# Kernel tuning notes

Hardware: AMD Instinct MI355X
Metric: run time of the kernel (lower is better)

Reference implementation:

```python
import jax, jax.numpy as jnp
import numpy as np

N = 8192      # nodes
IN_FEATS = 128
OUT_FEATS = 64
DEG = 16      # avg degree for random edges
NEG_SLOPE = 0.01  # nn.LeakyReLU default


def setup_inputs() -> dict:
    key = jax.random.key(0)
    k1, k2, k3, k4, k5, k6 = jax.random.split(key, 6)
    inputs = jax.random.normal(k1, (N, IN_FEATS), dtype=jnp.float32)
    # Random symmetric adjacency with self-loops (dense, as in the original module)
    us = jax.random.randint(k2, (N * DEG,), 0, N)
    vs = jax.random.randint(k3, (N * DEG,), 0, N)
    A = jnp.zeros((N, N), dtype=jnp.float32)
    A = A.at[us, vs].set(1.0)
    A = A.at[vs, us].set(1.0)
    idx = jnp.arange(N)
    A = A.at[idx, idx].set(1.0)
    # Linear layer params (torch nn.Linear: weight [out, in])
    W = jax.random.normal(k4, (OUT_FEATS, IN_FEATS), dtype=jnp.float32) * (1.0 / np.sqrt(IN_FEATS))
    b = jnp.zeros((OUT_FEATS,), dtype=jnp.float32)
    # attention params, torch.rand -> uniform [0,1)
    a1 = jax.random.uniform(k5, (1, OUT_FEATS), dtype=jnp.float32)
    a2 = jax.random.uniform(k6, (1, OUT_FEATS), dtype=jnp.float32)
    return {"inputs": inputs, "A": A, "W": W, "b": b, "a1": a1, "a2": a2}


def reference(inputs, A, W, b, a1, a2):
    z = inputs @ W.T + b                                  # [N, out]
    zi = jnp.sum(a1 * z, axis=1, keepdims=True)           # [N, 1]
    zj = jnp.sum(a2 * z, axis=1, keepdims=True)           # [N, 1]
    n = A.shape[0]
    idx = jnp.arange(n)
    diagA = jnp.diagonal(A)                               # A_ii
    # attention_A + attention_B = A*zi + diag(A_ii * zj)  (A*(eye*zj) only keeps diagonal)
    att = A * zi
    att = att.at[idx, idx].add(diagA * zj[:, 0])
    att = jax.nn.leaky_relu(att, NEG_SLOPE)
    att = jnp.exp(att) * A
    att = att / jnp.sum(att, axis=1, keepdims=True)       # row-normalize
    h = z - att @ z
    return jax.nn.relu(h)
```

## Files before the change

### kernel.cpp

```cpp
#include <hip/hip_runtime.h>
#include <math.h>

#define NN 8192
#define IN_F 128
#define OUT_F 64
#define NEG_SLOPE 0.01f
#define K1_ROWS 8
#define CAP 256

__global__ __launch_bounds__(256, 4) void k1_linear(
    const float* __restrict__ X, const float* __restrict__ W,
    const float* __restrict__ b, const float* __restrict__ a1,
    const float* __restrict__ a2, float* __restrict__ z,
    float* __restrict__ ev, float* __restrict__ dv)
{
    __shared__ float Wl[OUT_F * 129];
    __shared__ float xs[K1_ROWS * IN_F];
    const int t = threadIdx.x;
    const int blk = blockIdx.x;

    for (int idx = t; idx < OUT_F * IN_F; idx += 256) {
        int f = idx >> 7, k = idx & 127;
        Wl[f * 129 + k] = W[idx];
    }
    {
        const float4* Xv = reinterpret_cast<const float4*>(X + (size_t)blk * (K1_ROWS * IN_F));
        float4* xsv = reinterpret_cast<float4*>(xs);
        if (t < K1_ROWS * IN_F / 4) xsv[t] = Xv[t];
    }
    __syncthreads();

    const int wid = t >> 6;
    const int lane = t & 63;
    const float bias = b[lane];
    const float a1f = a1[lane], a2f = a2[lane];

#pragma unroll
    for (int r2 = 0; r2 < 2; ++r2) {
        const int row = wid * 2 + r2;
        float acc = 0.f;
#pragma unroll 8
        for (int k = 0; k < IN_F; ++k)
            acc = fmaf(xs[row * IN_F + k], Wl[lane * 129 + k], acc);
        const float zval = acc + bias;
        const int i = blk * K1_ROWS + row;
        z[i * OUT_F + lane] = zval;

        float p1 = a1f * zval;
        float p2 = a2f * zval;
#pragma unroll
        for (int off = 32; off > 0; off >>= 1) {
            p1 += __shfl_down(p1, off, 64);
            p2 += __shfl_down(p2, off, 64);
        }
        if (lane == 0) {
            const float s1 = p1;
            const float s2 = p1 + p2;
            const float l1 = s1 > 0.f ? s1 : NEG_SLOPE * s1;
            const float l2 = s2 > 0.f ? s2 : NEG_SLOPE * s2;
            ev[i] = expf(l1);
            dv[i] = expf(l2);
        }
    }
}

__global__ __launch_bounds__(256, 8) void k2a_compress(
    const float* __restrict__ A, int* __restrict__ degi, int* __restrict__ nbr)
{
    __shared__ int lst[CAP];
    __shared__ int cnt;
    const int i = blockIdx.x;
    const int t = threadIdx.x;
    if (t == 0) cnt = 0;
    __syncthreads();

    const int4* __restrict__ Arow =
        reinterpret_cast<const int4*>(A + (size_t)i * NN);

    int4 b0 = Arow[0 * 256 + t];
    int4 b1 = Arow[1 * 256 + t];
    int4 b2 = Arow[2 * 256 + t];
    int4 b3 = Arow[3 * 256 + t];
    int4 b4 = Arow[4 * 256 + t];
    int4 b5 = Arow[5 * 256 + t];
    int4 b6 = Arow[6 * 256 + t];
    int4 b7 = Arow[7 * 256 + t];

#define STEP(S, B)                                                           \
    {                                                                        \
        const int base = ((S) * 256 + t) * 4;                                \
        if (B.x != 0) { int k = atomicAdd(&cnt, 1); if (k < CAP) lst[k] = base;     } \
        if (B.y != 0) { int k = atomicAdd(&cnt, 1); if (k < CAP) lst[k] = base + 1; } \
        if (B.z != 0) { int k = atomicAdd(&cnt, 1); if (k < CAP) lst[k] = base + 2; } \
        if (B.w != 0) { int k = atomicAdd(&cnt, 1); if (k < CAP) lst[k] = base + 3; } \
    }
    STEP(0, b0) STEP(1, b1) STEP(2, b2) STEP(3, b3)
    STEP(4, b4) STEP(5, b5) STEP(6, b6) STEP(7, b7)
#undef STEP

    __syncthreads();
    const int c = cnt;
    if (t == 0) degi[i] = c;
    if (t < c && t < CAP) nbr[(size_t)i * CAP + t] = lst[t];
}

__global__ __launch_bounds__(256, 8) void k2b_gather(
    const int* __restrict__ degi, const int* __restrict__ nbr,
    const float* __restrict__ z, const float* __restrict__ ev,
    const float* __restrict__ dv, float* __restrict__ out)
{
    const int t = threadIdx.x;
    const int wid = t >> 6, lane = t & 63;
    const int i = blockIdx.x * 4 + wid;

    const int cnt = degi[i];
    const int* rowl = nbr + (size_t)i * CAP;

    float acc = 0.f;
    for (int k0 = 0; k0 < cnt; k0 += 64) {
        const int m = (cnt - k0) < 64 ? (cnt - k0) : 64;
        const int jv = (lane < m) ? rowl[k0 + lane] : 0;
        int kk = 0;
        for (; kk + 4 <= m; kk += 4) {
            const int j0 = __shfl(jv, kk + 0, 64);
            const int j1 = __shfl(jv, kk + 1, 64);
            const int j2 = __shfl(jv, kk + 2, 64);
            const int j3 = __shfl(jv, kk + 3, 64);
            const float z0 = z[(size_t)j0 * OUT_F + lane];
            const float z1 = z[(size_t)j1 * OUT_F + lane];
            const float z2 = z[(size_t)j2 * OUT_F + lane];
            const float z3 = z[(size_t)j3 * OUT_F + lane];
            acc += (z0 + z1) + (z2 + z3);
        }
        for (; kk < m; ++kk) {
            const int j = __shfl(jv, kk, 64);
            acc += z[(size_t)j * OUT_F + lane];
        }
    }

    const float degT = (float)cnt;
    const float e = ev[i], d = dv[i];
    const float S = (degT - 1.f) * e + d;
    const float zif = z[(size_t)i * OUT_F + lane];
    const float h = zif * (1.f + (e - d) / S) - (e / S) * acc;
    out[(size_t)i * OUT_F + lane] = h > 0.f ? h : 0.f;
}

extern "C" void kernel_launch(void* const* d_in, const int* in_sizes, int n_in,
                              void* d_out, int out_size, void* d_ws, size_t ws_size,
                              hipStream_t stream) {
    const float* X  = (const float*)d_in[0];
    const float* A  = (const float*)d_in[1];
    const float* W  = (const float*)d_in[2];
    const float* b  = (const float*)d_in[3];
    const float* a1 = (const float*)d_in[4];
    const float* a2 = (const float*)d_in[5];
    float* out = (float*)d_out;

    char* ws = (char*)d_ws;
    float* z    = (float*)ws;
    float* ev   = (float*)(ws + (size_t)NN * OUT_F * 4);
    float* dv   = ev + NN;
    int*   degi = (int*)(dv + NN);
    int*   nbr  = degi + NN;

    k1_linear<<<NN / K1_ROWS, 256, 0, stream>>>(X, W, b, a1, a2, z, ev, dv);
    k2a_compress<<<NN, 256, 0, stream>>>(A, degi, nbr);
    k2b_gather<<<NN / 4, 256, 0, stream>>>(degi, nbr, z, ev, dv, out);
}
```

Before: 64.84 us.

## Fuse linear projection into adjacency compression kernel and use nontemporal A loads

Merges the linear layer and attention-scalar computation into the per-row adjacency compression kernel, so each block computes one row of z, split across four waves with a shared-memory reduction, while its A row loads are in flight. This drops a kernel launch and a serialisation point, hiding the small GEMM under the memory-bound scan of the dense 256 MB adjacency. A is now read with nontemporal loads to avoid polluting cache. In exchange, every block reloads its slice of W from global/L2, and launch bounds drop from 8 to 4 blocks per CU, which may reduce the occupancy available to the streaming loads.

```diff
diff --git a/kernel.cpp b/kernel.cpp
--- a/kernel.cpp
+++ b/kernel.cpp
@@ -5,49 +5,82 @@
 #define IN_F 128
 #define OUT_F 64
 #define NEG_SLOPE 0.01f
-#define K1_ROWS 8
 #define CAP 256
 
-__global__ __launch_bounds__(256, 4) void k1_linear(
-    const float* __restrict__ X, const float* __restrict__ W,
-    const float* __restrict__ b, const float* __restrict__ a1,
-    const float* __restrict__ a2, float* __restrict__ z,
-    float* __restrict__ ev, float* __restrict__ dv)
+typedef int v4i __attribute__((ext_vector_type(4)));
+
+__global__ __launch_bounds__(256, 4) void k2a_fused(
+    const float* __restrict__ A, const float* __restrict__ X,
+    const float* __restrict__ W, const float* __restrict__ b,
+    const float* __restrict__ a1, const float* __restrict__ a2,
+    float* __restrict__ z, float* __restrict__ ev, float* __restrict__ dv,
+    int* __restrict__ degi, int* __restrict__ nbr)
 {
-    __shared__ float Wl[OUT_F * 129];
-    __shared__ float xs[K1_ROWS * IN_F];
+    __shared__ float xs[IN_F];
+    __shared__ float pz[4][64];
+    __shared__ int lst[CAP];
+    __shared__ int cnt;
+
+    const int i = blockIdx.x;
     const int t = threadIdx.x;
-    const int blk = blockIdx.x;
+    const int wid = t >> 6, lane = t & 63;
 
-    for (int idx = t; idx < OUT_F * IN_F; idx += 256) {
-        int f = idx >> 7, k = idx & 127;
-        Wl[f * 129 + k] = W[idx];
-    }
-    {
-        const float4* Xv = reinterpret_cast<const float4*>(X + (size_t)blk * (K1_ROWS * IN_F));
-        float4* xsv = reinterpret_cast<float4*>(xs);
-        if (t < K1_ROWS * IN_F / 4) xsv[t] = Xv[t];
-    }
+    if (t == 0) cnt = 0;
+    if (t < 32)
+        reinterpret_cast<float4*>(xs)[t] =
+            reinterpret_cast<const float4*>(X + (size_t)i * IN_F)[t];
+
+    const float4* wp4 = reinterpret_cast<const float4*>(W) + (lane * 32 + wid * 8);
+    float4 w4[8];
+#pragma unroll
+    for (int q = 0; q < 8; ++q) w4[q] = wp4[q];
+
     __syncthreads();
 
-    const int wid = t >> 6;
-    const int lane = t & 63;
-    const float bias = b[lane];
-    const float a1f = a1[lane], a2f = a2[lane];
+    const v4i* __restrict__ Arow = reinterpret_cast<const v4i*>(A + (size_t)i * NN);
+    v4i b0 = __builtin_nontemporal_load(&Arow[0 * 256 + t]);
+    v4i b1 = __builtin_nontemporal_load(&Arow[1 * 256 + t]);
+    v4i b2 = __builtin_nontemporal_load(&Arow[2 * 256 + t]);
+    v4i b3 = __builtin_nontemporal_load(&Arow[3 * 256 + t]);
+    v4i b4 = __builtin_nontemporal_load(&Arow[4 * 256 + t]);
+    v4i b5 = __builtin_nontemporal_load(&Arow[5 * 256 + t]);
+    v4i b6 = __builtin_nontemporal_load(&Arow[6 * 256 + t]);
+    v4i b7 = __builtin_nontemporal_load(&Arow[7 * 256 + t]);
 
+    {
+        float zp = 0.f;
+        const float* xq = xs + wid * 32;
 #pragma unroll
-    for (int r2 = 0; r2 < 2; ++r2) {
-        const int row = wid * 2 + r2;
-        float acc = 0.f;
-#pragma unroll 8
-        for (int k = 0; k < IN_F; ++k)
-            acc = fmaf(xs[row * IN_F + k], Wl[lane * 129 + k], acc);
-        const float zval = acc + bias;
-        const int i = blk * K1_ROWS + row;
-        z[i * OUT_F + lane] = zval;
+        for (int q = 0; q < 8; ++q) {
+            const float4 wv = w4[q];
+            zp = fmaf(wv.x, xq[q * 4 + 0], zp);
+            zp = fmaf(wv.y, xq[q * 4 + 1], zp);
+            zp = fmaf(wv.z, xq[q * 4 + 2], zp);
+            zp = fmaf(wv.w, xq[q * 4 + 3], zp);
+        }
+        pz[wid][lane] = zp;
+    }
 
-        float p1 = a1f * zval;
-        float p2 = a2f * zval;
+#define STEP(S, B)                                                              \
+    {                                                                           \
+        const int base = ((S) * 256 + t) * 4;                                   \
+        if (B.x != 0) { int k = atomicAdd(&cnt, 1); if (k < CAP) lst[k] = base;     } \
+        if (B.y != 0) { int k = atomicAdd(&cnt, 1); if (k < CAP) lst[k] = base + 1; } \
+        if (B.z != 0) { int k = atomicAdd(&cnt, 1); if (k < CAP) lst[k] = base + 2; } \
+        if (B.w != 0) { int k = atomicAdd(&cnt, 1); if (k < CAP) lst[k] = base + 3; } \
+    }
+    STEP(0, b0) STEP(1, b1) STEP(2, b2) STEP(3, b3)
+    STEP(4, b4) STEP(5, b5) STEP(6, b6) STEP(7, b7)
+#undef STEP
+
+    __syncthreads();
+
+    if (wid == 0) {
+        const float zv = pz[0][lane] + pz[1][lane] + pz[2][lane] + pz[3][lane]
+                       + b[lane];
+        z[(size_t)i * OUT_F + lane] = zv;
+        float p1 = a1[lane] * zv;
+        float p2 = a2[lane] * zv;
 #pragma unroll
         for (int off = 32; off > 0; off >>= 1) {
             p1 += __shfl_down(p1, off, 64);
@@ -62,43 +95,6 @@
             dv[i] = expf(l2);
         }
     }
-}
-
-__global__ __launch_bounds__(256, 8) void k2a_compress(
-    const float* __restrict__ A, int* __restrict__ degi, int* __restrict__ nbr)
-{
-    __shared__ int lst[CAP];
-    __shared__ int cnt;
-    const int i = blockIdx.x;
-    const int t = threadIdx.x;
-    if (t == 0) cnt = 0;
-    __syncthreads();
-
-    const int4* __restrict__ Arow =
-        reinterpret_cast<const int4*>(A + (size_t)i * NN);
-
-    int4 b0 = Arow[0 * 256 + t];
-    int4 b1 = Arow[1 * 256 + t];
-    int4 b2 = Arow[2 * 256 + t];
-    int4 b3 = Arow[3 * 256 + t];
-    int4 b4 = Arow[4 * 256 + t];
-    int4 b5 = Arow[5 * 256 + t];
-    int4 b6 = Arow[6 * 256 + t];
-    int4 b7 = Arow[7 * 256 + t];
-
-#define STEP(S, B)                                                           \
-    {                                                                        \
-        const int base = ((S) * 256 + t) * 4;                                \
-        if (B.x != 0) { int k = atomicAdd(&cnt, 1); if (k < CAP) lst[k] = base;     } \
-        if (B.y != 0) { int k = atomicAdd(&cnt, 1); if (k < CAP) lst[k] = base + 1; } \
-        if (B.z != 0) { int k = atomicAdd(&cnt, 1); if (k < CAP) lst[k] = base + 2; } \
-        if (B.w != 0) { int k = atomicAdd(&cnt, 1); if (k < CAP) lst[k] = base + 3; } \
-    }
-    STEP(0, b0) STEP(1, b1) STEP(2, b2) STEP(3, b3)
-    STEP(4, b4) STEP(5, b5) STEP(6, b6) STEP(7, b7)
-#undef STEP
-
-    __syncthreads();
     const int c = cnt;
     if (t == 0) degi[i] = c;
     if (t < c && t < CAP) nbr[(size_t)i * CAP + t] = lst[t];
@@ -164,7 +160,6 @@
     int*   degi = (int*)(dv + NN);
     int*   nbr  = degi + NN;
 
-    k1_linear<<<NN / K1_ROWS, 256, 0, stream>>>(X, W, b, a1, a2, z, ev, dv);
-    k2a_compress<<<NN, 256, 0, stream>>>(A, degi, nbr);
+    k2a_fused<<<NN, 256, 0, stream>>>(A, X, W, b, a1, a2, z, ev, dv, degi, nbr);
     k2b_gather<<<NN / 4, 256, 0, stream>>>(degi, nbr, z, ev, dv, out);
 }
```

After: 70.59 us. 1.09x slower.
